# Performance work log

Hardware: AMD Instinct MI355X
Metric: run time of the kernel (lower is better)

The kernel has to match this reference:

```python
import jax, jax.numpy as jnp
import numpy as np

NEG_SLOPE = 0.2
DROP_RATE = 0.1


def _spmm(rows, cols, vals, x):
    # sparse [N,N] @ dense [N,D] via gather + segment-sum
    n = x.shape[0]
    return jax.ops.segment_sum(vals[:, None] * x[cols], rows, num_segments=n)


def _dropout(x, key, rate=DROP_RATE):
    keep = 1.0 - rate
    mask = jax.random.bernoulli(key, keep, x.shape)
    return jnp.where(mask, x / keep, 0.0).astype(x.dtype)


def _leaky(x):
    return jnp.where(x >= 0, x, NEG_SLOPE * x)


def setup_inputs() -> dict:
    key = jax.random.key(0)
    N, HID, IEMB, NNZ = 100000, 256, 128, 3200000
    ks = jax.random.split(key, 8)
    x_idx = jnp.arange(N, dtype=jnp.int32)
    embed_weight = jax.random.normal(ks[0], (N, HID), jnp.float32) * 0.02
    G_rows = jax.random.randint(ks[1], (NNZ,), 0, N, jnp.int32)
    G_cols = jax.random.randint(ks[2], (NNZ,), 0, N, jnp.int32)
    G_vals = jax.random.uniform(ks[3], (NNZ,), jnp.float32) / 32.0
    W1 = jax.random.normal(ks[4], (HID, HID), jnp.float32) * (1.0 / np.sqrt(HID))
    b1 = jnp.zeros((HID,), jnp.float32)
    W2 = jax.random.normal(ks[5], (HID, HID), jnp.float32) * (1.0 / np.sqrt(HID))
    b2 = jnp.zeros((HID,), jnp.float32)
    W3 = jax.random.normal(ks[6], (IEMB, HID), jnp.float32) * (1.0 / np.sqrt(HID))
    b3 = jnp.zeros((IEMB,), jnp.float32)
    return {"x_idx": x_idx, "embed_weight": embed_weight,
            "G_rows": G_rows, "G_cols": G_cols, "G_vals": G_vals,
            "W1": W1, "b1": b1, "W2": W2, "b2": b2, "W3": W3, "b3": b3}


def reference(x_idx, embed_weight, G_rows, G_cols, G_vals, W1, b1, W2, b2, W3, b3):
    dk = jax.random.split(jax.random.key(42), 3)
    x = embed_weight[x_idx]                                   # [N, HID]
    m1 = _dropout(_spmm(G_rows, G_cols, G_vals, x) + x, dk[0])
    x1 = _leaky(m1 @ W1.T + b1)
    m2 = _dropout(_spmm(G_rows, G_cols, G_vals, x1) + x1, dk[1])
    x2 = _leaky(m2 @ W2.T + b2)
    m3 = _dropout(_spmm(G_rows, G_cols, G_vals, x2) + x2, dk[2])
    x3 = _leaky(m3 @ W3.T + b3)
    return jnp.concatenate((x, x1, x2, x3), axis=1)          # [N, 3*HID+IEMB]
```

## Files before the change

kernel.cpp:

```cpp
#include <hip/hip_runtime.h>
#include <stdint.h>
#include <stddef.h>

static constexpr int N    = 100000;
static constexpr int HID  = 256;
static constexpr int IEMB = 128;
static constexpr int NNZ  = 3200000;
static constexpr int OUTW = 3 * HID + IEMB;
static constexpr float NEG_SLOPE = 0.2f;

#define THREEFRY_PARTITIONABLE 1

typedef __attribute__((ext_vector_type(8))) short bf16x8;
typedef __attribute__((ext_vector_type(4))) float f32x4;
typedef __attribute__((ext_vector_type(4))) unsigned short us4;

__host__ __device__ inline uint32_t rotl32(uint32_t v, int r) {
  return (v << r) | (v >> (32 - r));
}

__host__ __device__ inline void threefry2x32(uint32_t k0, uint32_t k1,
                                             uint32_t x0, uint32_t x1,
                                             uint32_t& o0, uint32_t& o1) {
  const uint32_t k2 = k0 ^ k1 ^ 0x1BD11BDAu;
  x0 += k0; x1 += k1;
  x0 += x1; x1 = rotl32(x1, 13); x1 ^= x0;
  x0 += x1; x1 = rotl32(x1, 15); x1 ^= x0;
  x0 += x1; x1 = rotl32(x1, 26); x1 ^= x0;
  x0 += x1; x1 = rotl32(x1,  6); x1 ^= x0;
  x0 += k1; x1 += k2 + 1u;
  x0 += x1; x1 = rotl32(x1, 17); x1 ^= x0;
  x0 += x1; x1 = rotl32(x1, 29); x1 ^= x0;
  x0 += x1; x1 = rotl32(x1, 16); x1 ^= x0;
  x0 += x1; x1 = rotl32(x1, 24); x1 ^= x0;
  x0 += k2; x1 += k0 + 2u;
  x0 += x1; x1 = rotl32(x1, 13); x1 ^= x0;
  x0 += x1; x1 = rotl32(x1, 15); x1 ^= x0;
  x0 += x1; x1 = rotl32(x1, 26); x1 ^= x0;
  x0 += x1; x1 = rotl32(x1,  6); x1 ^= x0;
  x0 += k0; x1 += k1 + 3u;
  x0 += x1; x1 = rotl32(x1, 17); x1 ^= x0;
  x0 += x1; x1 = rotl32(x1, 29); x1 ^= x0;
  x0 += x1; x1 = rotl32(x1, 16); x1 ^= x0;
  x0 += x1; x1 = rotl32(x1, 24); x1 ^= x0;
  x0 += k1; x1 += k2 + 4u;
  x0 += x1; x1 = rotl32(x1, 13); x1 ^= x0;
  x0 += x1; x1 = rotl32(x1, 15); x1 ^= x0;
  x0 += x1; x1 = rotl32(x1, 26); x1 ^= x0;
  x0 += x1; x1 = rotl32(x1,  6); x1 ^= x0;
  x0 += k2; x1 += k0 + 5u;
  o0 = x0; o1 = x1;
}

__device__ inline bool keep_elem(uint32_t k0, uint32_t k1, uint32_t e) {
  uint32_t o0, o1, bits;
#if THREEFRY_PARTITIONABLE
  threefry2x32(k0, k1, 0u, e, o0, o1);
  bits = o0 ^ o1;
#else
  const uint32_t H = (uint32_t)(N) * (uint32_t)(HID) / 2u;
  if (e < H) { threefry2x32(k0, k1, e, e + H, o0, o1); bits = o0; }
  else       { threefry2x32(k0, k1, e - H, e, o0, o1); bits = o1; }
#endif
  float u = __uint_as_float((bits >> 9) | 0x3f800000u) - 1.0f;
  return u < 0.9f;
}

__device__ inline unsigned short f2bf_rne(float x) {
  uint32_t u = __float_as_uint(x);
  uint32_t r = (u + 0x7FFFu + ((u >> 16) & 1u)) >> 16;
  return (unsigned short)r;
}
__device__ inline float bf2f(unsigned short h) {
  return __uint_as_float(((uint32_t)h) << 16);
}


__global__ __launch_bounds__(256) void k_gather(const int* __restrict__ xidx,
                                                const float* __restrict__ emb,
                                                float* __restrict__ A,
                                                float* __restrict__ out) {
  int t = blockIdx.x * 256 + threadIdx.x;
  int n = t >> 6;
  int c4 = (t & 63) * 4;
  if (n >= N) return;
  int src = xidx[n];
  float4 v = *(const float4*)(emb + (size_t)src * HID + c4);
  *(float4*)(out + (size_t)n * OUTW + c4) = v;
  *(float4*)(A + (size_t)n * HID + c4) = v;
}

__global__ __launch_bounds__(256) void k_zero(float4* __restrict__ p, int n4) {
  int i = blockIdx.x * 256 + threadIdx.x;
  if (i < n4) p[i] = make_float4(0.f, 0.f, 0.f, 0.f);
}

__global__ __launch_bounds__(256) void k_zero_i(int* __restrict__ p, int n) {
  int i = blockIdx.x * 256 + threadIdx.x;
  if (i < n) p[i] = 0;
}

__global__ __launch_bounds__(256) void k_wsplit(const float* __restrict__ W,
                                                unsigned short* __restrict__ whi,
                                                unsigned short* __restrict__ wlo,
                                                int n) {
  int i = blockIdx.x * 256 + threadIdx.x;
  if (i >= n) return;
  float w = W[i];
  unsigned short h = f2bf_rne(w);
  unsigned short l = f2bf_rne(w - bf2f(h));
  whi[i] = h; wlo[i] = l;
}


__global__ __launch_bounds__(256) void k_hist(const int* __restrict__ rows,
                                              int* __restrict__ RO) {
  int e = blockIdx.x * 256 + threadIdx.x;
  if (e < NNZ) atomicAdd(&RO[rows[e]], 1);
}

__global__ __launch_bounds__(256) void k_scan(int* __restrict__ RO, int* __restrict__ C) {
  __shared__ int part[256];
  const int T = 256;
  const int K = (N + T - 1) / T;
  int t = threadIdx.x;
  int lo = t * K;
  int hi = lo + K; if (hi > N) hi = N;
  int s = 0;
  for (int i = lo; i < hi; ++i) s += RO[i];
  part[t] = s;
  __syncthreads();
  if (t == 0) {
    int run = 0;
    for (int i = 0; i < T; ++i) { int v = part[i]; part[i] = run; run += v; }
  }
  __syncthreads();
  int run = part[t];
  for (int i = lo; i < hi; ++i) {
    int v = RO[i];
    RO[i] = run;
    C[i]  = run;
    run += v;
  }
  if (t == T - 1) RO[N] = run;
}

__global__ __launch_bounds__(256) void k_scatter(const int* __restrict__ rows,
                                                 const int* __restrict__ cols,
                                                 const float* __restrict__ vals,
                                                 int* __restrict__ C,
                                                 int2* __restrict__ CV) {
  int e = blockIdx.x * 256 + threadIdx.x;
  if (e >= NNZ) return;
  int r = rows[e];
  int pos = atomicAdd(&C[r], 1);
  CV[pos] = make_int2(cols[e], __float_as_int(vals[e]));
}

__global__ __launch_bounds__(256) void k_spmm_csr(const int* __restrict__ RO,
                                                  const int2* __restrict__ CV,
                                                  const float* __restrict__ A,
                                                  float* __restrict__ B,
                                                  uint32_t k0, uint32_t k1) {
  int r = blockIdx.x * 4 + (threadIdx.x >> 6);
  if (r >= N) return;
  int c4 = (threadIdx.x & 63) * 4;
  int beg = RO[r], end = RO[r + 1];

  float ax = 0.f, ay = 0.f, az = 0.f, aw = 0.f;
  int i = beg;
  for (; i + 3 < end; i += 4) {
    int2 cv0 = CV[i + 0], cv1 = CV[i + 1], cv2 = CV[i + 2], cv3 = CV[i + 3];
    float4 x0 = *(const float4*)(A + (size_t)cv0.x * HID + c4);
    float4 x1 = *(const float4*)(A + (size_t)cv1.x * HID + c4);
    float4 x2 = *(const float4*)(A + (size_t)cv2.x * HID + c4);
    float4 x3 = *(const float4*)(A + (size_t)cv3.x * HID + c4);
    float v0 = __int_as_float(cv0.y), v1 = __int_as_float(cv1.y);
    float v2 = __int_as_float(cv2.y), v3 = __int_as_float(cv3.y);
    ax = fmaf(v0, x0.x, ax); ay = fmaf(v0, x0.y, ay);
    az = fmaf(v0, x0.z, az); aw = fmaf(v0, x0.w, aw);
    ax = fmaf(v1, x1.x, ax); ay = fmaf(v1, x1.y, ay);
    az = fmaf(v1, x1.z, az); aw = fmaf(v1, x1.w, aw);
    ax = fmaf(v2, x2.x, ax); ay = fmaf(v2, x2.y, ay);
    az = fmaf(v2, x2.z, az); aw = fmaf(v2, x2.w, aw);
    ax = fmaf(v3, x3.x, ax); ay = fmaf(v3, x3.y, ay);
    az = fmaf(v3, x3.z, az); aw = fmaf(v3, x3.w, aw);
  }
  for (; i < end; ++i) {
    int2 cv = CV[i];
    float v = __int_as_float(cv.y);
    float4 x = *(const float4*)(A + (size_t)cv.x * HID + c4);
    ax = fmaf(v, x.x, ax); ay = fmaf(v, x.y, ay);
    az = fmaf(v, x.z, az); aw = fmaf(v, x.w, aw);
  }

  float4 res = *(const float4*)(A + (size_t)r * HID + c4);
  uint32_t e0 = (uint32_t)r * (uint32_t)HID + (uint32_t)c4;
  float4 o;
  o.x = keep_elem(k0, k1, e0 + 0u) ? (ax + res.x) / 0.9f : 0.0f;
  o.y = keep_elem(k0, k1, e0 + 1u) ? (ay + res.y) / 0.9f : 0.0f;
  o.z = keep_elem(k0, k1, e0 + 2u) ? (az + res.z) / 0.9f : 0.0f;
  o.w = keep_elem(k0, k1, e0 + 3u) ? (aw + res.w) / 0.9f : 0.0f;
  *(float4*)(B + (size_t)r * HID + c4) = o;
}

template <int NC, bool WRITE_F32>
__global__ __launch_bounds__(256) void k_gemm_mfma(const float* __restrict__ M,
                                                   const unsigned short* __restrict__ Whi,
                                                   const unsigned short* __restrict__ Wlo,
                                                   const float* __restrict__ bias,
                                                   float* __restrict__ Aout,
                                                   float* __restrict__ out,
                                                   int colbase) {
  constexpr int WC = NC / 4;
  constexpr int CT = WC / 16;
  __shared__ __align__(16) unsigned short mhi[64 * 128];
  __shared__ __align__(16) unsigned short mlo[64 * 128];

  const int tid  = threadIdx.x;
  const int wave = tid >> 6;
  const int lane = tid & 63;
  const int l15  = lane & 15;
  const int lhi  = lane >> 4;
  const int row0 = blockIdx.x * 64;
  const int wc0  = wave * WC;

  const f32x4 fzero = {0.f, 0.f, 0.f, 0.f};
  f32x4 acc[4][CT];
#pragma unroll
  for (int rt = 0; rt < 4; ++rt)
#pragma unroll
    for (int ct = 0; ct < CT; ++ct) acc[rt][ct] = fzero;

  const int tk = (tid & 31) * 4;
  const int tr = tid >> 5;

#pragma unroll 1
  for (int kc = 0; kc < HID; kc += 128) {
    __syncthreads();
#pragma unroll
    for (int p = 0; p < 8; ++p) {
      int r = p * 8 + tr;
      int grow = row0 + r;
      float4 v = make_float4(0.f, 0.f, 0.f, 0.f);
      if (grow < N) v = *(const float4*)(M + (size_t)grow * HID + kc + tk);
      float vv[4] = {v.x, v.y, v.z, v.w};
      us4 h, l;
#pragma unroll
      for (int c = 0; c < 4; ++c) {
        unsigned short hh = f2bf_rne(vv[c]);
        h[c] = hh;
        l[c] = f2bf_rne(vv[c] - bf2f(hh));
      }
      int sidx = r * 128 + (tk ^ ((r & 7) << 3));
      *(us4*)(&mhi[sidx]) = h;
      *(us4*)(&mlo[sidx]) = l;
    }
    __syncthreads();

#pragma unroll
    for (int ks = 0; ks < 128; ks += 32) {
      const int kf = ks + lhi * 8;
      bf16x8 ah[4], al[4];
#pragma unroll
      for (int rt = 0; rt < 4; ++rt) {
        int r = rt * 16 + l15;
        int idx = r * 128 + (kf ^ ((r & 7) << 3));
        ah[rt] = *(const bf16x8*)(&mhi[idx]);
        al[rt] = *(const bf16x8*)(&mlo[idx]);
      }
#pragma unroll
      for (int ct = 0; ct < CT; ++ct) {
        int col = wc0 + ct * 16 + l15;
        const unsigned short* wph = Whi + (size_t)col * HID + kc + kf;
        const unsigned short* wpl = Wlo + (size_t)col * HID + kc + kf;
        bf16x8 bh = *(const bf16x8*)wph;
        bf16x8 bl = *(const bf16x8*)wpl;
#pragma unroll
        for (int rt = 0; rt < 4; ++rt) {
          acc[rt][ct] = __builtin_amdgcn_mfma_f32_16x16x32_bf16(ah[rt], bh, acc[rt][ct], 0, 0, 0);
          acc[rt][ct] = __builtin_amdgcn_mfma_f32_16x16x32_bf16(ah[rt], bl, acc[rt][ct], 0, 0, 0);
          acc[rt][ct] = __builtin_amdgcn_mfma_f32_16x16x32_bf16(al[rt], bh, acc[rt][ct], 0, 0, 0);
        }
      }
    }
  }

#pragma unroll
  for (int ct = 0; ct < CT; ++ct) {
    int col = wc0 + ct * 16 + l15;
    float bv = bias[col];
#pragma unroll
    for (int rt = 0; rt < 4; ++rt) {
#pragma unroll
      for (int rg = 0; rg < 4; ++rg) {
        int grow = row0 + rt * 16 + lhi * 4 + rg;
        if (grow < N) {
          float v = acc[rt][ct][rg] + bv;
          v = (v >= 0.f) ? v : NEG_SLOPE * v;
          out[(size_t)grow * OUTW + colbase + col] = v;
          if (WRITE_F32) Aout[(size_t)grow * HID + col] = v;
        }
      }
    }
  }
}

__global__ __launch_bounds__(256) void k_spmm(const int* __restrict__ rows,
                                              const int* __restrict__ cols,
                                              const float* __restrict__ vals,
                                              const float* __restrict__ A,
                                              float* __restrict__ B) {
  int e = blockIdx.x * 4 + (threadIdx.x >> 6);
  int lane = threadIdx.x & 63;
  if (e >= NNZ) return;
  int r = rows[e];
  int c = cols[e];
  float v = vals[e];
  float4 x = *(const float4*)(A + (size_t)c * HID + lane * 4);
  float* bp = B + (size_t)r * HID + lane * 4;
  unsafeAtomicAdd(bp + 0, v * x.x);
  unsafeAtomicAdd(bp + 1, v * x.y);
  unsafeAtomicAdd(bp + 2, v * x.z);
  unsafeAtomicAdd(bp + 3, v * x.w);
}

__global__ __launch_bounds__(256) void k_dropres(const float* __restrict__ A,
                                                 float* __restrict__ B,
                                                 uint32_t k0, uint32_t k1) {
  uint32_t e = blockIdx.x * 256 + threadIdx.x;
  if (e >= (uint32_t)N * HID) return;
  float m = B[e] + A[e];
  B[e] = keep_elem(k0, k1, e) ? (m / 0.9f) : 0.0f;
}

template <int NC, bool WRITE_F32>
__global__ __launch_bounds__(256) void k_gemm(const float* __restrict__ M,
                                              const float* __restrict__ W,
                                              const float* __restrict__ bias,
                                              float* __restrict__ Aout,
                                              float* __restrict__ out,
                                              int colbase) {
  constexpr int CG = NC / 4;
  constexpr int RG = 256 / CG;
  constexpr int RPT = 64 / RG;
  __shared__ float m_s[64][68];

  const int tid = threadIdx.x;
  const int j = tid % CG;
  const int rg = tid / CG;
  const int row0 = blockIdx.x * 64;
  const int r0 = rg * RPT;

  float acc[RPT][4];
#pragma unroll
  for (int i = 0; i < RPT; ++i)
#pragma unroll
    for (int c = 0; c < 4; ++c) acc[i][c] = 0.f;

  const int rr = tid >> 4;
  const int kk = (tid & 15) * 4;

#pragma unroll 1
  for (int kc = 0; kc < HID; kc += 64) {
    __syncthreads();
#pragma unroll
    for (int p = 0; p < 4; ++p) {
      int r = p * 16 + rr;
      int grow = row0 + r;
      float4 v = make_float4(0.f, 0.f, 0.f, 0.f);
      if (grow < N) v = *(const float4*)(M + (size_t)grow * HID + kc + kk);
      m_s[kk + 0][r] = v.x;
      m_s[kk + 1][r] = v.y;
      m_s[kk + 2][r] = v.z;
      m_s[kk + 3][r] = v.w;
    }
    __syncthreads();

#pragma unroll 1
    for (int ks = 0; ks < 64; ks += 8) {
      float4 wa[4], wb[4];
#pragma unroll
      for (int c = 0; c < 4; ++c) {
        const float* wp = W + (size_t)(4 * j + c) * HID + kc + ks;
        wa[c] = *(const float4*)(wp);
        wb[c] = *(const float4*)(wp + 4);
      }
#pragma unroll
      for (int q = 0; q < 8; ++q) {
        float wf[4];
#pragma unroll
        for (int c = 0; c < 4; ++c) {
          const float* wv = (q < 4) ? (const float*)&wa[c] : (const float*)&wb[c];
          wf[c] = wv[q & 3];
        }
        const float* ms = &m_s[ks + q][r0];
#pragma unroll
        for (int ii = 0; ii < RPT / 4; ++ii) {
          float4 mv = *(const float4*)(ms + ii * 4);
          const float mr[4] = {mv.x, mv.y, mv.z, mv.w};
#pragma unroll
          for (int t = 0; t < 4; ++t)
#pragma unroll
            for (int c = 0; c < 4; ++c)
              acc[ii * 4 + t][c] = fmaf(mr[t], wf[c], acc[ii * 4 + t][c]);
        }
      }
    }
  }

  float bv[4];
#pragma unroll
  for (int c = 0; c < 4; ++c) bv[c] = bias[4 * j + c];

#pragma unroll
  for (int i = 0; i < RPT; ++i) {
    int grow = row0 + r0 + i;
    if (grow < N) {
      float4 ov;
      float* ovp = (float*)&ov;
#pragma unroll
      for (int c = 0; c < 4; ++c) {
        float v = acc[i][c] + bv[c];
        ovp[c] = (v >= 0.f) ? v : NEG_SLOPE * v;
      }
      if (WRITE_F32)
        *(float4*)(Aout + (size_t)grow * HID + 4 * j) = ov;
      *(float4*)(out + (size_t)grow * OUTW + colbase + 4 * j) = ov;
    }
  }
}

extern "C" void kernel_launch(void* const* d_in, const int* in_sizes, int n_in,
                              void* d_out, int out_size, void* d_ws, size_t ws_size,
                              hipStream_t stream) {
  (void)in_sizes; (void)n_in; (void)out_size;

  const int*   x_idx  = (const int*)d_in[0];
  const float* emb    = (const float*)d_in[1];
  const int*   g_rows = (const int*)d_in[2];
  const int*   g_cols = (const int*)d_in[3];
  const float* g_vals = (const float*)d_in[4];
  const float* W1 = (const float*)d_in[5];
  const float* b1 = (const float*)d_in[6];
  const float* W2 = (const float*)d_in[7];
  const float* b2 = (const float*)d_in[8];
  const float* W3 = (const float*)d_in[9];
  const float* b3 = (const float*)d_in[10];
  float* out = (float*)d_out;

  float* A = (float*)d_ws;
  float* B = A + (size_t)N * HID;
  int*   RO = (int*)(B + (size_t)N * HID);
  int*   C  = RO + (N + 2);
  int2*  CV = (int2*)(C + N);
  uintptr_t wsp = ((uintptr_t)(CV + NNZ) + 63) & ~(uintptr_t)63;
  unsigned short* Wh0 = (unsigned short*)wsp;
  unsigned short* Wl0 = Wh0 + 65536;
  unsigned short* Wh1 = Wl0 + 65536;
  unsigned short* Wl1 = Wh1 + 65536;
  unsigned short* Wh2 = Wl1 + 65536;
  unsigned short* Wl2 = Wh2 + 32768;
  const size_t NEED = (size_t)N * HID * 2 * sizeof(float)
                    + (size_t)(N + 2 + N) * sizeof(int)
                    + (size_t)NNZ * sizeof(int2)
                    + 64
                    + (size_t)(4 * 65536 + 2 * 32768) * sizeof(unsigned short);
  const bool use_csr = (ws_size >= NEED);

  uint32_t dk[3][2];
#if THREEFRY_PARTITIONABLE
  for (uint32_t i = 0; i < 3; ++i)
    threefry2x32(0u, 42u, 0u, i, dk[i][0], dk[i][1]);
#else
  {
    uint32_t a0, c0, a1, c1, a2, c2;
    threefry2x32(0u, 42u, 0u, 3u, a0, c0);
    threefry2x32(0u, 42u, 1u, 4u, a1, c1);
    threefry2x32(0u, 42u, 2u, 5u, a2, c2);
    dk[0][0] = a0; dk[0][1] = a1;
    dk[1][0] = a2; dk[1][1] = c0;
    dk[2][0] = c1; dk[2][1] = c2;
  }
#endif

  const int gemm_blocks = (N + 63) / 64;

  k_gather<<<(N * 64) / 256, 256, 0, stream>>>(x_idx, emb, A, out);

  const float* Ws[3] = {W1, W2, W3};
  const float* bs[3] = {b1, b2, b3};
  unsigned short* Whs[3] = {Wh0, Wh1, Wh2};
  unsigned short* Wls[3] = {Wl0, Wl1, Wl2};

  if (use_csr) {
    k_zero_i<<<(N + 2 + 255) / 256, 256, 0, stream>>>(RO, N + 2);
    k_hist<<<(NNZ + 255) / 256, 256, 0, stream>>>(g_rows, RO);
    k_scan<<<1, 256, 0, stream>>>(RO, C);
    k_scatter<<<(NNZ + 255) / 256, 256, 0, stream>>>(g_rows, g_cols, g_vals, C, CV);
    k_wsplit<<<(65536 + 255) / 256, 256, 0, stream>>>(W1, Wh0, Wl0, 65536);
    k_wsplit<<<(65536 + 255) / 256, 256, 0, stream>>>(W2, Wh1, Wl1, 65536);
    k_wsplit<<<(32768 + 255) / 256, 256, 0, stream>>>(W3, Wh2, Wl2, 32768);
  }

  for (int l = 0; l < 3; ++l) {
    if (use_csr) {
      k_spmm_csr<<<(N + 3) / 4, 256, 0, stream>>>(RO, CV, A, B, dk[l][0], dk[l][1]);
      if (l < 2)
        k_gemm_mfma<HID, true><<<gemm_blocks, 256, 0, stream>>>(B, Whs[l], Wls[l], bs[l], A, out, HID * (l + 1));
      else
        k_gemm_mfma<IEMB, false><<<gemm_blocks, 256, 0, stream>>>(B, Whs[2], Wls[2], bs[2], nullptr, out, 3 * HID);
    } else {
      k_zero<<<(N * HID / 4 + 255) / 256, 256, 0, stream>>>((float4*)B, N * HID / 4);
      k_spmm<<<NNZ / 4, 256, 0, stream>>>(g_rows, g_cols, g_vals, A, B);
      k_dropres<<<(N * HID) / 256, 256, 0, stream>>>(A, B, dk[l][0], dk[l][1]);
      if (l < 2)
        k_gemm<HID, true><<<gemm_blocks, 256, 0, stream>>>(B, Ws[l], bs[l], A, out, HID * (l + 1));
      else
        k_gemm<IEMB, false><<<gemm_blocks, 256, 0, stream>>>(B, Ws[2], bs[2], nullptr, out, 3 * HID);
    }
  }
}
```

Before: 2.785 ms.

## Gather SpMM neighbor rows from a bf16 shadow copy of activations

Keeps a bf16 copy of the activation matrix, written by the gather and GEMM epilogues, and has the CSR SpMM read neighbor rows from that copy instead of fp32. This halves the bytes fetched by the random-access neighbor gathers, which dominate SpMM memory traffic. The main loop is unrolled to 8 edges with loads batched first, and the dropout mask is computed before the loop. The cost is extra bf16 writes, more workspace, and reduced precision in the aggregated neighbor sums.

Result: faster. 2.277 ms (-18.2%).

```diff
diff --git a/kernel.cpp b/kernel.cpp
--- a/kernel.cpp
+++ b/kernel.cpp
@@ -79,6 +79,7 @@
 __global__ __launch_bounds__(256) void k_gather(const int* __restrict__ xidx,
                                                 const float* __restrict__ emb,
                                                 float* __restrict__ A,
+                                                unsigned short* __restrict__ Abf,
                                                 float* __restrict__ out) {
   int t = blockIdx.x * 256 + threadIdx.x;
   int n = t >> 6;
@@ -88,6 +89,12 @@
   float4 v = *(const float4*)(emb + (size_t)src * HID + c4);
   *(float4*)(out + (size_t)n * OUTW + c4) = v;
   *(float4*)(A + (size_t)n * HID + c4) = v;
+  if (Abf) {
+    us4 q;
+    q[0] = f2bf_rne(v.x); q[1] = f2bf_rne(v.y);
+    q[2] = f2bf_rne(v.z); q[3] = f2bf_rne(v.w);
+    *(us4*)(Abf + (size_t)n * HID + c4) = q;
+  }
 }
 
 __global__ __launch_bounds__(256) void k_zero(float4* __restrict__ p, int n4) {
@@ -157,9 +164,11 @@
   CV[pos] = make_int2(cols[e], __float_as_int(vals[e]));
 }
 
+template <bool BF>
 __global__ __launch_bounds__(256) void k_spmm_csr(const int* __restrict__ RO,
                                                   const int2* __restrict__ CV,
                                                   const float* __restrict__ A,
+                                                  const unsigned short* __restrict__ Abf,
                                                   float* __restrict__ B,
                                                   uint32_t k0, uint32_t k1) {
   int r = blockIdx.x * 4 + (threadIdx.x >> 6);
@@ -167,40 +176,77 @@
   int c4 = (threadIdx.x & 63) * 4;
   int beg = RO[r], end = RO[r + 1];
 
+  float4 res = *(const float4*)(A + (size_t)r * HID + c4);
+  uint32_t e0 = (uint32_t)r * (uint32_t)HID + (uint32_t)c4;
+  bool kp0 = keep_elem(k0, k1, e0 + 0u);
+  bool kp1 = keep_elem(k0, k1, e0 + 1u);
+  bool kp2 = keep_elem(k0, k1, e0 + 2u);
+  bool kp3 = keep_elem(k0, k1, e0 + 3u);
+
   float ax = 0.f, ay = 0.f, az = 0.f, aw = 0.f;
   int i = beg;
-  for (; i + 3 < end; i += 4) {
-    int2 cv0 = CV[i + 0], cv1 = CV[i + 1], cv2 = CV[i + 2], cv3 = CV[i + 3];
-    float4 x0 = *(const float4*)(A + (size_t)cv0.x * HID + c4);
-    float4 x1 = *(const float4*)(A + (size_t)cv1.x * HID + c4);
-    float4 x2 = *(const float4*)(A + (size_t)cv2.x * HID + c4);
-    float4 x3 = *(const float4*)(A + (size_t)cv3.x * HID + c4);
-    float v0 = __int_as_float(cv0.y), v1 = __int_as_float(cv1.y);
-    float v2 = __int_as_float(cv2.y), v3 = __int_as_float(cv3.y);
-    ax = fmaf(v0, x0.x, ax); ay = fmaf(v0, x0.y, ay);
-    az = fmaf(v0, x0.z, az); aw = fmaf(v0, x0.w, aw);
-    ax = fmaf(v1, x1.x, ax); ay = fmaf(v1, x1.y, ay);
-    az = fmaf(v1, x1.z, az); aw = fmaf(v1, x1.w, aw);
-    ax = fmaf(v2, x2.x, ax); ay = fmaf(v2, x2.y, ay);
-    az = fmaf(v2, x2.z, az); aw = fmaf(v2, x2.w, aw);
-    ax = fmaf(v3, x3.x, ax); ay = fmaf(v3, x3.y, ay);
-    az = fmaf(v3, x3.z, az); aw = fmaf(v3, x3.w, aw);
-  }
-  for (; i < end; ++i) {
-    int2 cv = CV[i];
-    float v = __int_as_float(cv.y);
-    float4 x = *(const float4*)(A + (size_t)cv.x * HID + c4);
-    ax = fmaf(v, x.x, ax); ay = fmaf(v, x.y, ay);
-    az = fmaf(v, x.z, az); aw = fmaf(v, x.w, aw);
-  }
-
-  float4 res = *(const float4*)(A + (size_t)r * HID + c4);
-  uint32_t e0 = (uint32_t)r * (uint32_t)HID + (uint32_t)c4;
+
+  if (BF) {
+#pragma unroll 1
+    for (; i + 7 < end; i += 8) {
+      int2 cv[8];
+#pragma unroll
+      for (int u = 0; u < 8; ++u) cv[u] = CV[i + u];
+      us4 q[8];
+#pragma unroll
+      for (int u = 0; u < 8; ++u)
+        q[u] = *(const us4*)(Abf + (size_t)cv[u].x * HID + c4);
+#pragma unroll
+      for (int u = 0; u < 8; ++u) {
+        float v = __int_as_float(cv[u].y);
+        ax = fmaf(v, bf2f(q[u][0]), ax);
+        ay = fmaf(v, bf2f(q[u][1]), ay);
+        az = fmaf(v, bf2f(q[u][2]), az);
+        aw = fmaf(v, bf2f(q[u][3]), aw);
+      }
+    }
+    for (; i < end; ++i) {
+      int2 cv = CV[i];
+      float v = __int_as_float(cv.y);
+      us4 q = *(const us4*)(Abf + (size_t)cv.x * HID + c4);
+      ax = fmaf(v, bf2f(q[0]), ax);
+      ay = fmaf(v, bf2f(q[1]), ay);
+      az = fmaf(v, bf2f(q[2]), az);
+      aw = fmaf(v, bf2f(q[3]), aw);
+    }
+  } else {
+#pragma unroll 1
+    for (; i + 3 < end; i += 4) {
+      int2 cv0 = CV[i + 0], cv1 = CV[i + 1], cv2 = CV[i + 2], cv3 = CV[i + 3];
+      float4 x0 = *(const float4*)(A + (size_t)cv0.x * HID + c4);
+      float4 x1 = *(const float4*)(A + (size_t)cv1.x * HID + c4);
+      float4 x2 = *(const float4*)(A + (size_t)cv2.x * HID + c4);
+      float4 x3 = *(const float4*)(A + (size_t)cv3.x * HID + c4);
+      float v0 = __int_as_float(cv0.y), v1 = __int_as_float(cv1.y);
+      float v2 = __int_as_float(cv2.y), v3 = __int_as_float(cv3.y);
+      ax = fmaf(v0, x0.x, ax); ay = fmaf(v0, x0.y, ay);
+      az = fmaf(v0, x0.z, az); aw = fmaf(v0, x0.w, aw);
+      ax = fmaf(v1, x1.x, ax); ay = fmaf(v1, x1.y, ay);
+      az = fmaf(v1, x1.z, az); aw = fmaf(v1, x1.w, aw);
+      ax = fmaf(v2, x2.x, ax); ay = fmaf(v2, x2.y, ay);
+      az = fmaf(v2, x2.z, az); aw = fmaf(v2, x2.w, aw);
+      ax = fmaf(v3, x3.x, ax); ay = fmaf(v3, x3.y, ay);
+      az = fmaf(v3, x3.z, az); aw = fmaf(v3, x3.w, aw);
+    }
+    for (; i < end; ++i) {
+      int2 cv = CV[i];
+      float v = __int_as_float(cv.y);
+      float4 x = *(const float4*)(A + (size_t)cv.x * HID + c4);
+      ax = fmaf(v, x.x, ax); ay = fmaf(v, x.y, ay);
+      az = fmaf(v, x.z, az); aw = fmaf(v, x.w, aw);
+    }
+  }
+
   float4 o;
-  o.x = keep_elem(k0, k1, e0 + 0u) ? (ax + res.x) / 0.9f : 0.0f;
-  o.y = keep_elem(k0, k1, e0 + 1u) ? (ay + res.y) / 0.9f : 0.0f;
-  o.z = keep_elem(k0, k1, e0 + 2u) ? (az + res.z) / 0.9f : 0.0f;
-  o.w = keep_elem(k0, k1, e0 + 3u) ? (aw + res.w) / 0.9f : 0.0f;
+  o.x = kp0 ? (ax + res.x) / 0.9f : 0.0f;
+  o.y = kp1 ? (ay + res.y) / 0.9f : 0.0f;
+  o.z = kp2 ? (az + res.z) / 0.9f : 0.0f;
+  o.w = kp3 ? (aw + res.w) / 0.9f : 0.0f;
   *(float4*)(B + (size_t)r * HID + c4) = o;
 }
 
@@ -210,6 +256,7 @@
                                                    const unsigned short* __restrict__ Wlo,
                                                    const float* __restrict__ bias,
                                                    float* __restrict__ Aout,
+                                                   unsigned short* __restrict__ Abf,
                                                    float* __restrict__ out,
                                                    int colbase) {
   constexpr int WC = NC / 4;
@@ -299,7 +346,10 @@
           float v = acc[rt][ct][rg] + bv;
           v = (v >= 0.f) ? v : NEG_SLOPE * v;
           out[(size_t)grow * OUTW + colbase + col] = v;
-          if (WRITE_F32) Aout[(size_t)grow * HID + col] = v;
+          if (WRITE_F32) {
+            Aout[(size_t)grow * HID + col] = v;
+            if (Abf) Abf[(size_t)grow * HID + col] = f2bf_rne(v);
+          }
         }
       }
     }
@@ -461,12 +511,16 @@
   unsigned short* Wl1 = Wh1 + 65536;
   unsigned short* Wh2 = Wl1 + 65536;
   unsigned short* Wl2 = Wh2 + 32768;
-  const size_t NEED = (size_t)N * HID * 2 * sizeof(float)
-                    + (size_t)(N + 2 + N) * sizeof(int)
-                    + (size_t)NNZ * sizeof(int2)
-                    + 64
-                    + (size_t)(4 * 65536 + 2 * 32768) * sizeof(unsigned short);
-  const bool use_csr = (ws_size >= NEED);
+  unsigned short* Abf = Wl2 + 32768;
+  const size_t NEED_CSR = (size_t)N * HID * 2 * sizeof(float)
+                        + (size_t)(N + 2 + N) * sizeof(int)
+                        + (size_t)NNZ * sizeof(int2)
+                        + 64
+                        + (size_t)(4 * 65536 + 2 * 32768) * sizeof(unsigned short);
+  const size_t NEED_BF = NEED_CSR + (size_t)N * HID * sizeof(unsigned short);
+  const bool use_csr = (ws_size >= NEED_CSR);
+  const bool use_bf  = (ws_size >= NEED_BF);
+  unsigned short* AbfArg = use_bf ? Abf : nullptr;
 
   uint32_t dk[3][2];
 #if THREEFRY_PARTITIONABLE
@@ -486,7 +540,7 @@
 
   const int gemm_blocks = (N + 63) / 64;
 
-  k_gather<<<(N * 64) / 256, 256, 0, stream>>>(x_idx, emb, A, out);
+  k_gather<<<(N * 64) / 256, 256, 0, stream>>>(x_idx, emb, A, AbfArg, out);
 
   const float* Ws[3] = {W1, W2, W3};
   const float* bs[3] = {b1, b2, b3};
@@ -505,11 +559,14 @@
 
   for (int l = 0; l < 3; ++l) {
     if (use_csr) {
-      k_spmm_csr<<<(N + 3) / 4, 256, 0, stream>>>(RO, CV, A, B, dk[l][0], dk[l][1]);
+      if (use_bf)
+        k_spmm_csr<true><<<(N + 3) / 4, 256, 0, stream>>>(RO, CV, A, Abf, B, dk[l][0], dk[l][1]);
+      else
+        k_spmm_csr<false><<<(N + 3) / 4, 256, 0, stream>>>(RO, CV, A, nullptr, B, dk[l][0], dk[l][1]);
       if (l < 2)
-        k_gemm_mfma<HID, true><<<gemm_blocks, 256, 0, stream>>>(B, Whs[l], Wls[l], bs[l], A, out, HID * (l + 1));
+        k_gemm_mfma<HID, true><<<gemm_blocks, 256, 0, stream>>>(B, Whs[l], Wls[l], bs[l], A, AbfArg, out, HID * (l + 1));
       else
-        k_gemm_mfma<IEMB, false><<<gemm_blocks, 256, 0, stream>>>(B, Whs[2], Wls[2], bs[2], nullptr, out, 3 * HID);
+        k_gemm_mfma<IEMB, false><<<gemm_blocks, 256, 0, stream>>>(B, Whs[2], Wls[2], bs[2], nullptr, nullptr, out, 3 * HID);
     } else {
       k_zero<<<(N * HID / 4 + 255) / 256, 256, 0, stream>>>((float4*)B, N * HID / 4);
       k_spmm<<<NNZ / 4, 256, 0, stream>>>(g_rows, g_cols, g_vals, A, B);
```
